# Kernel tuning notes

Hardware: AMD Instinct MI355X
Metric: run time of the kernel (lower is better)

The kernel has to match this reference:

```python
import jax, jax.numpy as jnp
import numpy as np

N = 10000        # nodes
E = 320000       # edges (avg degree 32)
W = 256          # width (assert width >= 256)
H = 8            # num_head (RESCALE_EDGE assumed (1,1) -> nhead=8, dhead=32)
D = W // H       # per-head dim
BOND = 33        # EMBED_BOND[0]
BAG = 3          # indices per edge bag
EPS_GN = 1e-5


def setup_inputs() -> dict:
    key = jax.random.key(0)
    ks = jax.random.split(key, 12)
    x = jax.random.normal(ks[0], (N, W), dtype=jnp.float32)
    edge_idx = jax.random.randint(ks[1], (2, E), 0, N)
    edge_attr = jax.random.randint(ks[2], (E, BAG), 0, BOND)
    # node in-degree wrt scatter target edge_idx[1], clamped to >= 1
    deg = jax.ops.segment_sum(jnp.ones((E,), jnp.float32), edge_idx[1], num_segments=N)
    deg = jnp.maximum(deg, 1.0)
    s = 1.0 / np.sqrt(W)
    W_src = jax.random.normal(ks[3], (W, W), dtype=jnp.float32) * s
    W_tgt = jax.random.normal(ks[4], (W, W), dtype=jnp.float32) * s
    emb = jax.random.normal(ks[5], (BOND, W), dtype=jnp.float32) * 0.02
    emb = emb.at[0].set(0.0)  # padding_idx=0 row is zeros
    sd = 1.0 / np.sqrt(D)
    W_gate = jax.random.normal(ks[6], (H, D, D), dtype=jnp.float32) * sd  # grouped conv1d k=1
    W_val = jax.random.normal(ks[7], (H, D, D), dtype=jnp.float32) * sd
    W_post = jax.random.normal(ks[8], (W, W), dtype=jnp.float32) * s
    deg_param = jnp.zeros((W,), jnp.float32) - 0.01  # DegreeLayer degree_init
    return {"x": x, "deg": deg, "edge_idx": edge_idx, "edge_attr": edge_attr,
            "W_src": W_src, "W_tgt": W_tgt, "emb": emb,
            "W_gate": W_gate, "W_val": W_val, "W_post": W_post,
            "deg_param": deg_param}


def reference(x, deg, edge_idx, edge_attr, W_src, W_tgt, emb, W_gate, W_val, W_post, deg_param):
    # src/tgt 1x1 Conv1d == per-node linear, then edge gather
    xs = x @ W_src.T                      # [N, W]
    xt = x @ W_tgt.T                      # [N, W]
    xx = xs[edge_idx[0]] + xt[edge_idx[1]]  # [E, W]

    # EmbeddingBag(mode='mean', padding_idx=0): padded entries excluded
    mask = (edge_attr != 0).astype(xx.dtype)            # [E, BAG]
    bag = jnp.einsum('ebc,eb->ec', emb[edge_attr], mask)  # [E, W]
    cnt = jnp.maximum(mask.sum(-1, keepdims=True), 1.0)
    gate_bias = bag / cnt

    # GroupNorm(H, W, affine=False) over [E, W, 1]
    xg = xx.reshape(-1, H, D)
    mu = xg.mean(-1, keepdims=True)
    var = xg.var(-1, keepdims=True)
    xn = (xg - mu) / jnp.sqrt(var + EPS_GN)              # [E, H, D]

    # gated grouped 1x1 convs (dropout is identity at eval)
    gin = xn + gate_bias.reshape(-1, H, D)
    gate = jax.nn.relu(jnp.einsum('ehd,hfd->ehf', gin, W_gate))
    val = jnp.einsum('ehd,hfd->ehf', xn, W_val)
    act = (gate * val).reshape(-1, W)                    # [E, W]
    out_e = act @ W_post.T                               # [E, W]

    # scatter-sum to nodes, then degree rescale
    agg = jax.ops.segment_sum(out_e, edge_idx[1], num_segments=x.shape[0])
    return jnp.power(deg[:, None], deg_param) * agg      # [N, W]
```

## Files before the change

kernel.cpp:

```cpp
#include <hip/hip_runtime.h>

#define WID 256
#define EPS_GN 1e-5f

typedef __bf16 v8bf __attribute__((ext_vector_type(8)));
typedef __bf16 v2bf __attribute__((ext_vector_type(2)));
typedef float  v4f  __attribute__((ext_vector_type(4)));

__device__ inline unsigned short f2b(float f) {
    unsigned int u = __builtin_bit_cast(unsigned int, f);
    unsigned int r = (u + 0x7fffu + ((u >> 16) & 1u)) >> 16;
    return (unsigned short)r;
}
__device__ inline float lo16(unsigned int u) { return __builtin_bit_cast(float, u << 16); }
__device__ inline float hi16(unsigned int u) { return __builtin_bit_cast(float, u & 0xffff0000u); }

#if __has_builtin(__builtin_amdgcn_cvt_pk_bf16_f32)
__device__ inline unsigned int pkbf(float a, float b) {
    v2bf r = __builtin_amdgcn_cvt_pk_bf16_f32(a, b);
    return __builtin_bit_cast(unsigned int, r);
}
#else
__device__ inline unsigned int pkbf(float a, float b) {
    return (unsigned int)f2b(a) | ((unsigned int)f2b(b) << 16);
}
#endif

#if __has_builtin(__builtin_amdgcn_fdot2_f32_bf16)
__device__ inline float pairsum(unsigned int u, float s) {
    v2bf p = __builtin_bit_cast(v2bf, u);
    v2bf ones = __builtin_bit_cast(v2bf, 0x3f803f80u);
    return __builtin_amdgcn_fdot2_f32_bf16(p, ones, s, false);
}
#else
__device__ inline float pairsum(unsigned int u, float s) {
    return s + lo16(u) + hi16(u);
}
#endif

__global__ void cast_k(const float* __restrict__ Wsrc, const float* __restrict__ Wtgt,
                       const float* __restrict__ Wp, const float* __restrict__ Wg,
                       const float* __restrict__ Wv, const float* __restrict__ emb,
                       unsigned short* __restrict__ Wsb, unsigned short* __restrict__ Wtb,
                       unsigned short* __restrict__ Wpb, unsigned short* __restrict__ Wgb,
                       unsigned short* __restrict__ Wvb, unsigned short* __restrict__ embWgT,
                       int* __restrict__ cnt, int N, int BOND) {
    int i = blockIdx.x * 256 + threadIdx.x;
    int gsz = gridDim.x * 256;
    for (int j = i; j < N; j += gsz) cnt[j] = 0;
    for (int j = i; j < 65536; j += gsz) {
        Wsb[j] = f2b(Wsrc[j]); Wtb[j] = f2b(Wtgt[j]); Wpb[j] = f2b(Wp[j]);
    }
    for (int j = i; j < 8192; j += gsz) { Wgb[j] = f2b(Wg[j]); Wvb[j] = f2b(Wv[j]); }
    for (int j = i; j < 16384; j += gsz) {
        int jr = j >> 6, k = j & 63;
        float sacc = 0.f;
        if (k < BOND) {
            int h = jr >> 5, f = jr & 31;
            const float* er = emb + (size_t)k * WID + h * 32;
            const float* wr = Wg + h * 1024 + f * 32;
#pragma unroll
            for (int d = 0; d < 32; d++) sacc += er[d] * wr[d];
        }
        embWgT[jr * 64 + k] = f2b(sacc);
    }
}

__global__ __launch_bounds__(256, 2)
void prepproj_k(const float* __restrict__ x, const unsigned short* __restrict__ Wsb,
                const unsigned short* __restrict__ Wtb, const int* __restrict__ eidx,
                unsigned short* __restrict__ xsb, unsigned short* __restrict__ xtb,
                int* __restrict__ cnt, float* __restrict__ aggact,
                int N, int E, int PB, int AUX) {
    __shared__ unsigned short ab[32 * 264];
    int t = threadIdx.x, b = blockIdx.x;

    if (b >= PB) {
        int atid = (b - PB) * 256 + t, asz = AUX * 256;
        {
            float4* ap = (float4*)aggact;
            int n4 = (N * WID) >> 2;
            for (int i = atid; i < n4; i += asz) ap[i] = make_float4(0.f, 0.f, 0.f, 0.f);
        }
        for (int i = atid; i < E; i += asz) atomicAdd(&cnt[eidx[E + i]], 1);
        return;
    }

    int n0 = b * 32;
#pragma unroll
    for (int ch = 0; ch < 8; ch++) {
        int flat = ch * 1024 + t * 4;
        int row = flat >> 8, col = flat & 255;
        int n = n0 + row;
        float4 v = (n < N) ? *(const float4*)&x[(size_t)n * WID + col]
                           : make_float4(0.f, 0.f, 0.f, 0.f);
        *(uint2*)&ab[row * 264 + col] = make_uint2(pkbf(v.x, v.y), pkbf(v.z, v.w));
    }
    __syncthreads();
    int w = t >> 6, lane = t & 63, m = lane & 15, kg = lane >> 4;
#pragma unroll
    for (int pass = 0; pass < 2; pass++) {
        const unsigned short* Wb = pass ? Wtb : Wsb;
        unsigned short* outp = pass ? xtb : xsb;
        v4f acc[2][4];
#pragma unroll
        for (int mt = 0; mt < 2; mt++)
#pragma unroll
            for (int nt = 0; nt < 4; nt++) acc[mt][nt] = (v4f){0.f, 0.f, 0.f, 0.f};
#pragma unroll
        for (int kt = 0; kt < 8; kt++) {
            int k0 = kt * 32 + kg * 8;
            v8bf a0 = *(const v8bf*)&ab[m * 264 + k0];
            v8bf a1 = *(const v8bf*)&ab[(16 + m) * 264 + k0];
#pragma unroll
            for (int nt = 0; nt < 4; nt++) {
                int j = w * 64 + nt * 16 + m;
                v8bf bfr = *(const v8bf*)&Wb[j * 256 + k0];
                acc[0][nt] = __builtin_amdgcn_mfma_f32_16x16x32_bf16(a0, bfr, acc[0][nt], 0, 0, 0);
                acc[1][nt] = __builtin_amdgcn_mfma_f32_16x16x32_bf16(a1, bfr, acc[1][nt], 0, 0, 0);
            }
        }
#pragma unroll
        for (int mt = 0; mt < 2; mt++)
#pragma unroll
            for (int r = 0; r < 4; r++) {
                int n = n0 + mt * 16 + kg * 4 + r;
                if (n < N)
#pragma unroll
                    for (int nt = 0; nt < 4; nt++)
                        outp[(size_t)n * WID + w * 64 + nt * 16 + m] = f2b(acc[mt][nt][r]);
            }
    }
}

__global__ void scan_k(const int* __restrict__ cnt, int* __restrict__ cur, int N) {
    __shared__ int buf[10240];
    __shared__ int part[1024];
    int t = threadIdx.x;
    int C = (N + 1023) >> 10;
    int M = C << 10;
    for (int i = t; i < M; i += 1024) buf[i] = (i < N) ? cnt[i] : 0;
    __syncthreads();
    int base0 = t * C;
    int s = 0;
    for (int i = 0; i < C; i++) s += buf[base0 + i];
    part[t] = s;
    __syncthreads();
    for (int d = 1; d < 1024; d <<= 1) {
        int v = (t >= d) ? part[t - d] : 0;
        __syncthreads();
        part[t] += v;
        __syncthreads();
    }
    int base = (t == 0) ? 0 : part[t - 1];
    for (int i = 0; i < C; i++) {
        int idx = base0 + i;
        int v = buf[idx];
        buf[idx] = base;
        base += v;
    }
    __syncthreads();
    for (int i = t; i < N; i += 1024) cur[i] = buf[i];
}

__global__ void scat_k(const int* __restrict__ eidx, int* __restrict__ cur,
                       int* __restrict__ perm, int E) {
    int i = blockIdx.x * 256 + threadIdx.x;
    if (i < E) { int p = atomicAdd(&cur[eidx[E + i]], 1); perm[p] = i; }
}

__global__ __launch_bounds__(256, 7)
void edge_k(const unsigned short* __restrict__ xsb, const unsigned short* __restrict__ xtb,
            const int* __restrict__ eidx, const int* __restrict__ eattr,
            const int* __restrict__ perm, const unsigned short* __restrict__ Wgb,
            const unsigned short* __restrict__ Wvb, const unsigned short* __restrict__ embWgT,
            float* __restrict__ aggact, int E, int NT, int PER) {
    __shared__ unsigned short xxb[8704];
    __shared__ unsigned short Mld[32 * 72];
    __shared__ int src_s[32], tgt_s[32];
    __shared__ int segmask_s;

    int tile = (blockIdx.x & 7) * PER + (blockIdx.x >> 3);
    if (tile >= NT) return;
    int t = threadIdx.x;
    int e0 = tile * 32;
    int ne = min(32, E - e0);

    {
        int tgtv = -1;
        if (t < 32) {
            int p = (t < ne) ? perm[e0 + t] : -1;
            src_s[t] = (p >= 0) ? eidx[p] : 0;
            tgtv = (p >= 0) ? eidx[E + p] : -1;
            tgt_s[t] = (tgtv >= 0) ? tgtv : 0;
            int a0 = 0, a1 = 0, a2 = 0;
            if (p >= 0) {
                const int* ap = eattr + (size_t)p * 3;
                a0 = ap[0]; a1 = ap[1]; a2 = ap[2];
            }
            unsigned int* Mr = (unsigned int*)&Mld[t * 72];
#pragma unroll
            for (int q = 0; q < 32; q++) Mr[q] = 0;
            int c = (a0 != 0) + (a1 != 0) + (a2 != 0);
            float inv = (p >= 0 && c > 0) ? 1.f / (float)c : 0.f;
            float wa = inv * (float)(1 + (a1 == a0) + (a2 == a0));
            float wb = inv * (float)(1 + (a2 == a1));
            Mld[t * 72 + a0] = f2b(wa);
            if (a1 != a0) Mld[t * 72 + a1] = f2b(wb);
            if (a2 != a0 && a2 != a1) Mld[t * 72 + a2] = f2b(inv);
        }
        if (t < 64) {
            int nxt = __shfl_down(tgtv, 1);
            bool flag = (t < ne) && ((t == ne - 1) || (nxt != tgtv));
            unsigned long long bal = __ballot(flag);
            if (t == 0) segmask_s = (int)(unsigned int)bal;
        }
    }
    __syncthreads();

    {
        int e = t >> 3, c = t & 7;
        int sn = src_s[e], g = tgt_s[e];
        bool live = (e < ne);
        const uint4* ps = (const uint4*)(xsb + (size_t)sn * WID);
        const uint4* pt = (const uint4*)(xtb + (size_t)g * WID);
        uint4 us[4], ut[4];
#pragma unroll
        for (int i = 0; i < 4; i++) { us[i] = ps[c + 8 * i]; ut[i] = pt[c + 8 * i]; }
        float v[4][8], sum[4], sq[4];
#pragma unroll
        for (int i = 0; i < 4; i++) {
            const unsigned int* au = (const unsigned int*)&us[i];
            const unsigned int* bu = (const unsigned int*)&ut[i];
            sum[i] = 0.f; sq[i] = 0.f;
#pragma unroll
            for (int q = 0; q < 4; q++) {
                float x0 = lo16(au[q]) + lo16(bu[q]);
                float x1 = hi16(au[q]) + hi16(bu[q]);
                if (!live) { x0 = 0.f; x1 = 0.f; }
                v[i][2 * q] = x0; v[i][2 * q + 1] = x1;
                sum[i] += x0 + x1;
                sq[i] += x0 * x0 + x1 * x1;
            }
        }
#pragma unroll
        for (int mask = 1; mask <= 2; mask <<= 1)
#pragma unroll
            for (int i = 0; i < 4; i++) {
                sum[i] += __shfl_xor(sum[i], mask);
                sq[i]  += __shfl_xor(sq[i], mask);
            }
#pragma unroll
        for (int i = 0; i < 4; i++) {
            float mu = sum[i] * (1.f / 32.f);
            float var = sq[i] * (1.f / 32.f) - mu * mu;
            float rs = rsqrtf(var + EPS_GN);
            float nmr = -mu * rs;
            unsigned int pk[4];
#pragma unroll
            for (int q = 0; q < 4; q++)
                pk[q] = pkbf(fmaf(v[i][2 * q], rs, nmr), fmaf(v[i][2 * q + 1], rs, nmr));
            *(uint4*)&xxb[e * 264 + (c + 8 * i) * 8] = make_uint4(pk[0], pk[1], pk[2], pk[3]);
        }
    }
    __syncthreads();

    {
        int w = t >> 6, lane = t & 63, m = lane & 15, kg = lane >> 4;
        v8bf axn[2][2], aM[2][2];
#pragma unroll
        for (int mt = 0; mt < 2; mt++) {
            int row = mt * 16 + m;
            axn[0][mt] = *(const v8bf*)&xxb[row * 264 + (w * 2 + 0) * 32 + kg * 8];
            axn[1][mt] = *(const v8bf*)&xxb[row * 264 + (w * 2 + 1) * 32 + kg * 8];
            aM[mt][0] = *(const v8bf*)&Mld[row * 72 + kg * 8];
            aM[mt][1] = *(const v8bf*)&Mld[row * 72 + 32 + kg * 8];
        }
        __syncthreads();
        v4f z = {0.f, 0.f, 0.f, 0.f};
#pragma unroll
        for (int hh = 0; hh < 2; hh++) {
            int h = w * 2 + hh;
#pragma unroll
            for (int nt = 0; nt < 2; nt++) {
                int fj = nt * 16 + m;
                int j = h * 32 + fj;
                v8bf bWg = *(const v8bf*)&Wgb[h * 1024 + fj * 32 + kg * 8];
                v8bf bWv = *(const v8bf*)&Wvb[h * 1024 + fj * 32 + kg * 8];
                v8bf bE0 = *(const v8bf*)&embWgT[j * 64 + kg * 8];
                v8bf bE1 = *(const v8bf*)&embWgT[j * 64 + 32 + kg * 8];
#pragma unroll
                for (int mt = 0; mt < 2; mt++) {
                    v4f cgm = __builtin_amdgcn_mfma_f32_16x16x32_bf16(axn[hh][mt], bWg, z, 0, 0, 0);
                    cgm = __builtin_amdgcn_mfma_f32_16x16x32_bf16(aM[mt][0], bE0, cgm, 0, 0, 0);
                    cgm = __builtin_amdgcn_mfma_f32_16x16x32_bf16(aM[mt][1], bE1, cgm, 0, 0, 0);
                    v4f cv = __builtin_amdgcn_mfma_f32_16x16x32_bf16(axn[hh][mt], bWv, z, 0, 0, 0);
                    float a0 = fmaxf(cgm[0], 0.f) * cv[0];
                    float a1 = fmaxf(cgm[1], 0.f) * cv[1];
                    float a2 = fmaxf(cgm[2], 0.f) * cv[2];
                    float a3 = fmaxf(cgm[3], 0.f) * cv[3];
                    int e0i = mt * 16 + kg * 4;
                    *(unsigned int*)&xxb[j * 34 + e0i]     = pkbf(a0, a1);
                    *(unsigned int*)&xxb[j * 34 + e0i + 2] = pkbf(a2, a3);
                }
            }
        }
    }
    __syncthreads();

    {
        unsigned int mask = (unsigned int)__builtin_amdgcn_readfirstlane(segmask_s);
        float sum = 0.f;
#pragma unroll
        for (int i = 0; i < 16; i++) {
            unsigned int r = *(const unsigned int*)&xxb[t * 34 + 2 * i];
            if (!((mask >> (2 * i)) & 1)) {
                sum = pairsum(r, sum);
                if ((mask >> (2 * i + 1)) & 1) {
                    int tg = __builtin_amdgcn_readfirstlane(tgt_s[2 * i + 1]);
                    atomicAdd(&aggact[(size_t)tg * WID + t], sum);
                    sum = 0.f;
                }
            } else {
                sum += lo16(r);
                int tg = __builtin_amdgcn_readfirstlane(tgt_s[2 * i]);
                atomicAdd(&aggact[(size_t)tg * WID + t], sum);
                sum = hi16(r);
                if ((mask >> (2 * i + 1)) & 1) {
                    int tg2 = __builtin_amdgcn_readfirstlane(tgt_s[2 * i + 1]);
                    atomicAdd(&aggact[(size_t)tg2 * WID + t], sum);
                    sum = 0.f;
                }
            }
        }
    }
}

__global__ __launch_bounds__(256, 2)
void post_k(const float* __restrict__ aggact, const unsigned short* __restrict__ Wpb,
            const float* __restrict__ deg, const float* __restrict__ dp,
            float* __restrict__ out, int N) {
    __shared__ unsigned short ab[32 * 264];
    __shared__ float degl[32];
    int t = threadIdx.x;
    int n0 = blockIdx.x * 32;
#pragma unroll
    for (int ch = 0; ch < 8; ch++) {
        int flat = ch * 1024 + t * 4;
        int row = flat >> 8, col = flat & 255;
        int n = n0 + row;
        float4 v = (n < N) ? *(const float4*)&aggact[(size_t)n * WID + col]
                           : make_float4(0.f, 0.f, 0.f, 0.f);
        *(uint2*)&ab[row * 264 + col] = make_uint2(pkbf(v.x, v.y), pkbf(v.z, v.w));
    }
    if (t < 32) {
        int n = n0 + t;
        degl[t] = (n < N) ? log2f(deg[n]) : 0.f;
    }
    __syncthreads();
    int w = t >> 6, lane = t & 63, m = lane & 15, kg = lane >> 4;
    v4f acc[2][4];
#pragma unroll
    for (int mt = 0; mt < 2; mt++)
#pragma unroll
        for (int nt = 0; nt < 4; nt++) acc[mt][nt] = (v4f){0.f, 0.f, 0.f, 0.f};
#pragma unroll
    for (int kt = 0; kt < 8; kt++) {
        int k0 = kt * 32 + kg * 8;
        v8bf a0 = *(const v8bf*)&ab[m * 264 + k0];
        v8bf a1 = *(const v8bf*)&ab[(16 + m) * 264 + k0];
#pragma unroll
        for (int nt = 0; nt < 4; nt++) {
            int j = w * 64 + nt * 16 + m;
            v8bf b = *(const v8bf*)&Wpb[j * 256 + k0];
            acc[0][nt] = __builtin_amdgcn_mfma_f32_16x16x32_bf16(a0, b, acc[0][nt], 0, 0, 0);
            acc[1][nt] = __builtin_amdgcn_mfma_f32_16x16x32_bf16(a1, b, acc[1][nt], 0, 0, 0);
        }
    }
    float dpv[4];
#pragma unroll
    for (int nt = 0; nt < 4; nt++) dpv[nt] = dp[w * 64 + nt * 16 + m];
#pragma unroll
    for (int mt = 0; mt < 2; mt++)
#pragma unroll
        for (int r = 0; r < 4; r++) {
            int row = mt * 16 + kg * 4 + r;
            int n = n0 + row;
            if (n < N) {
                float ld = degl[row];
#pragma unroll
                for (int nt = 0; nt < 4; nt++)
                    out[(size_t)n * WID + w * 64 + nt * 16 + m] =
                        exp2f(dpv[nt] * ld) * acc[mt][nt][r];
            }
        }
}

extern "C" void kernel_launch(void* const* d_in, const int* in_sizes, int n_in,
                              void* d_out, int out_size, void* d_ws, size_t ws_size,
                              hipStream_t stream) {
    const float* x    = (const float*)d_in[0];
    const float* deg  = (const float*)d_in[1];
    const int*   eidx = (const int*)d_in[2];
    const int*   eatt = (const int*)d_in[3];
    const float* Wsrc = (const float*)d_in[4];
    const float* Wtgt = (const float*)d_in[5];
    const float* emb  = (const float*)d_in[6];
    const float* Wg   = (const float*)d_in[7];
    const float* Wv   = (const float*)d_in[8];
    const float* Wp   = (const float*)d_in[9];
    const float* dp   = (const float*)d_in[10];
    int N = in_sizes[0] / WID;
    int E = in_sizes[2] / 2;
    int BOND = in_sizes[6] / WID;

    float* ws     = (float*)d_ws;
    float* aggact = ws;
    int*   cnt    = (int*)(aggact + (size_t)N * WID);
    int*   cur    = cnt + N;
    int*   perm   = cur + N;
    unsigned short* xsb = (unsigned short*)(perm + E);
    unsigned short* xtb = xsb + (size_t)N * WID;
    unsigned short* Wsb = xtb + (size_t)N * WID;
    unsigned short* Wtb = Wsb + 65536;
    unsigned short* Wpb = Wtb + 65536;
    unsigned short* Wgb = Wpb + 65536;
    unsigned short* Wvb = Wgb + 8192;
    unsigned short* embWgT = Wvb + 8192;

    int PB = (N + 31) / 32;
    int AUX = 128;
    int NT = (E + 31) / 32;
    int PER = (NT + 7) / 8;

    cast_k<<<320, 256, 0, stream>>>(Wsrc, Wtgt, Wp, Wg, Wv, emb,
                                    Wsb, Wtb, Wpb, Wgb, Wvb, embWgT, cnt, N, BOND);
    prepproj_k<<<PB + AUX, 256, 0, stream>>>(x, Wsb, Wtb, eidx, xsb, xtb, cnt, aggact,
                                             N, E, PB, AUX);
    scan_k<<<1, 1024, 0, stream>>>(cnt, cur, N);
    scat_k<<<(E + 255) / 256, 256, 0, stream>>>(eidx, cur, perm, E);
    edge_k<<<PER * 8, 256, 0, stream>>>(xsb, xtb, eidx, eatt, perm, Wgb, Wvb, embWgT,
                                        aggact, E, NT, PER);
    post_k<<<(N + 31) / 32, 256, 0, stream>>>(aggact, Wpb, deg, dp, (float*)d_out, N);
}
```

Baseline: 230.3 us.

## Pre-sort edge data in scatter, fold bond embedding to 32 slots, vectorize stores

The scatter kernel now writes src, tgt and packed bag attributes directly in target-sorted order, so the edge kernel reads them contiguously instead of chasing a permutation through the edge arrays. The bond-embedding projection table is folded from 64 to 32 columns by aliasing index 32 to slot 0 (the padding slot), which drops one MFMA per gate tile and halves the embedding LDS tile. The projection and post GEMMs swap their MFMA operands so each lane holds four consecutive columns, giving packed 8-byte bf16 and float4 output stores. Occupancy is raised to 8 and the pad edges are zeroed in setup. The fold depends on BOND being at most 33, and pad edges now rely on zeroed buffers instead of the old liveness masking.

```diff
diff --git a/kernel.cpp b/kernel.cpp
--- a/kernel.cpp
+++ b/kernel.cpp
@@ -44,25 +44,29 @@
                        unsigned short* __restrict__ Wsb, unsigned short* __restrict__ Wtb,
                        unsigned short* __restrict__ Wpb, unsigned short* __restrict__ Wgb,
                        unsigned short* __restrict__ Wvb, unsigned short* __restrict__ embWgT,
-                       int* __restrict__ cnt, int N, int BOND) {
+                       int* __restrict__ cnt, int* __restrict__ ssrc,
+                       int* __restrict__ stgt, int* __restrict__ sattr,
+                       int N, int BOND, int E, int NT32) {
     int i = blockIdx.x * 256 + threadIdx.x;
     int gsz = gridDim.x * 256;
     for (int j = i; j < N; j += gsz) cnt[j] = 0;
+    for (int j = E + i; j < NT32; j += gsz) { ssrc[j] = 0; stgt[j] = 0; sattr[j] = 0; }
     for (int j = i; j < 65536; j += gsz) {
         Wsb[j] = f2b(Wsrc[j]); Wtb[j] = f2b(Wtgt[j]); Wpb[j] = f2b(Wp[j]);
     }
     for (int j = i; j < 8192; j += gsz) { Wgb[j] = f2b(Wg[j]); Wvb[j] = f2b(Wv[j]); }
-    for (int j = i; j < 16384; j += gsz) {
-        int jr = j >> 6, k = j & 63;
+    for (int j = i; j < 8192; j += gsz) {
+        int jr = j >> 5, k = j & 31;
+        int kk = k ? k : 32;
         float sacc = 0.f;
-        if (k < BOND) {
+        if (kk < BOND) {
             int h = jr >> 5, f = jr & 31;
-            const float* er = emb + (size_t)k * WID + h * 32;
+            const float* er = emb + (size_t)kk * WID + h * 32;
             const float* wr = Wg + h * 1024 + f * 32;
 #pragma unroll
             for (int d = 0; d < 32; d++) sacc += er[d] * wr[d];
         }
-        embWgT[jr * 64 + k] = f2b(sacc);
+        embWgT[jr * 32 + k] = f2b(sacc);
     }
 }
 
@@ -116,20 +120,23 @@
             for (int nt = 0; nt < 4; nt++) {
                 int j = w * 64 + nt * 16 + m;
                 v8bf bfr = *(const v8bf*)&Wb[j * 256 + k0];
-                acc[0][nt] = __builtin_amdgcn_mfma_f32_16x16x32_bf16(a0, bfr, acc[0][nt], 0, 0, 0);
-                acc[1][nt] = __builtin_amdgcn_mfma_f32_16x16x32_bf16(a1, bfr, acc[1][nt], 0, 0, 0);
-            }
-        }
-#pragma unroll
-        for (int mt = 0; mt < 2; mt++)
-#pragma unroll
-            for (int r = 0; r < 4; r++) {
-                int n = n0 + mt * 16 + kg * 4 + r;
-                if (n < N)
-#pragma unroll
-                    for (int nt = 0; nt < 4; nt++)
-                        outp[(size_t)n * WID + w * 64 + nt * 16 + m] = f2b(acc[mt][nt][r]);
-            }
+                acc[0][nt] = __builtin_amdgcn_mfma_f32_16x16x32_bf16(bfr, a0, acc[0][nt], 0, 0, 0);
+                acc[1][nt] = __builtin_amdgcn_mfma_f32_16x16x32_bf16(bfr, a1, acc[1][nt], 0, 0, 0);
+            }
+        }
+#pragma unroll
+        for (int mt = 0; mt < 2; mt++) {
+            int n = n0 + mt * 16 + m;
+            if (n < N) {
+#pragma unroll
+                for (int nt = 0; nt < 4; nt++) {
+                    int j0 = w * 64 + nt * 16 + kg * 4;
+                    *(uint2*)&outp[(size_t)n * WID + j0] =
+                        make_uint2(pkbf(acc[mt][nt][0], acc[mt][nt][1]),
+                                   pkbf(acc[mt][nt][2], acc[mt][nt][3]));
+                }
+            }
+        }
     }
 }
 
@@ -163,20 +170,28 @@
     for (int i = t; i < N; i += 1024) cur[i] = buf[i];
 }
 
-__global__ void scat_k(const int* __restrict__ eidx, int* __restrict__ cur,
-                       int* __restrict__ perm, int E) {
+__global__ void scat_k(const int* __restrict__ eidx, const int* __restrict__ eattr,
+                       int* __restrict__ cur, int* __restrict__ ssrc,
+                       int* __restrict__ stgt, int* __restrict__ sattr, int E) {
     int i = blockIdx.x * 256 + threadIdx.x;
-    if (i < E) { int p = atomicAdd(&cur[eidx[E + i]], 1); perm[p] = i; }
-}
-
-__global__ __launch_bounds__(256, 7)
+    if (i < E) {
+        int tg = eidx[E + i];
+        int p = atomicAdd(&cur[tg], 1);
+        ssrc[p] = eidx[i];
+        stgt[p] = tg;
+        const int* ap = eattr + (size_t)i * 3;
+        sattr[p] = (ap[0] & 63) | ((ap[1] & 63) << 6) | ((ap[2] & 63) << 12);
+    }
+}
+
+__global__ __launch_bounds__(256, 8)
 void edge_k(const unsigned short* __restrict__ xsb, const unsigned short* __restrict__ xtb,
-            const int* __restrict__ eidx, const int* __restrict__ eattr,
-            const int* __restrict__ perm, const unsigned short* __restrict__ Wgb,
+            const int* __restrict__ ssrc, const int* __restrict__ stgt,
+            const int* __restrict__ sattr, const unsigned short* __restrict__ Wgb,
             const unsigned short* __restrict__ Wvb, const unsigned short* __restrict__ embWgT,
             float* __restrict__ aggact, int E, int NT, int PER) {
     __shared__ unsigned short xxb[8704];
-    __shared__ unsigned short Mld[32 * 72];
+    __shared__ unsigned short Mld[32 * 40];
     __shared__ int src_s[32], tgt_s[32];
     __shared__ int segmask_s;
 
@@ -189,25 +204,23 @@
     {
         int tgtv = -1;
         if (t < 32) {
-            int p = (t < ne) ? perm[e0 + t] : -1;
-            src_s[t] = (p >= 0) ? eidx[p] : 0;
-            tgtv = (p >= 0) ? eidx[E + p] : -1;
-            tgt_s[t] = (tgtv >= 0) ? tgtv : 0;
-            int a0 = 0, a1 = 0, a2 = 0;
-            if (p >= 0) {
-                const int* ap = eattr + (size_t)p * 3;
-                a0 = ap[0]; a1 = ap[1]; a2 = ap[2];
-            }
-            unsigned int* Mr = (unsigned int*)&Mld[t * 72];
-#pragma unroll
-            for (int q = 0; q < 32; q++) Mr[q] = 0;
+            int e = e0 + t;
+            src_s[t] = ssrc[e];
+            int tg = stgt[e];
+            tgt_s[t] = tg;
+            int pa = sattr[e];
+            unsigned int* Mr = (unsigned int*)&Mld[t * 40];
+#pragma unroll
+            for (int q = 0; q < 16; q++) Mr[q] = 0;
+            int a0 = pa & 63, a1 = (pa >> 6) & 63, a2 = (pa >> 12) & 63;
             int c = (a0 != 0) + (a1 != 0) + (a2 != 0);
-            float inv = (p >= 0 && c > 0) ? 1.f / (float)c : 0.f;
+            float inv = (c > 0) ? 1.f / (float)c : 0.f;
             float wa = inv * (float)(1 + (a1 == a0) + (a2 == a0));
             float wb = inv * (float)(1 + (a2 == a1));
-            Mld[t * 72 + a0] = f2b(wa);
-            if (a1 != a0) Mld[t * 72 + a1] = f2b(wb);
-            if (a2 != a0 && a2 != a1) Mld[t * 72 + a2] = f2b(inv);
+            if (a0) Mld[t * 40 + (a0 & 31)] = f2b(wa);
+            if (a1 && a1 != a0) Mld[t * 40 + (a1 & 31)] = f2b(wb);
+            if (a2 && a2 != a0 && a2 != a1) Mld[t * 40 + (a2 & 31)] = f2b(inv);
+            tgtv = (t < ne) ? tg : -1;
         }
         if (t < 64) {
             int nxt = __shfl_down(tgtv, 1);
@@ -221,7 +234,6 @@
     {
         int e = t >> 3, c = t & 7;
         int sn = src_s[e], g = tgt_s[e];
-        bool live = (e < ne);
         const uint4* ps = (const uint4*)(xsb + (size_t)sn * WID);
         const uint4* pt = (const uint4*)(xtb + (size_t)g * WID);
         uint4 us[4], ut[4];
@@ -237,7 +249,6 @@
             for (int q = 0; q < 4; q++) {
                 float x0 = lo16(au[q]) + lo16(bu[q]);
                 float x1 = hi16(au[q]) + hi16(bu[q]);
-                if (!live) { x0 = 0.f; x1 = 0.f; }
                 v[i][2 * q] = x0; v[i][2 * q + 1] = x1;
                 sum[i] += x0 + x1;
                 sq[i] += x0 * x0 + x1 * x1;
@@ -267,14 +278,13 @@
 
     {
         int w = t >> 6, lane = t & 63, m = lane & 15, kg = lane >> 4;
-        v8bf axn[2][2], aM[2][2];
+        v8bf axn[2][2], aM[2];
 #pragma unroll
         for (int mt = 0; mt < 2; mt++) {
             int row = mt * 16 + m;
             axn[0][mt] = *(const v8bf*)&xxb[row * 264 + (w * 2 + 0) * 32 + kg * 8];
             axn[1][mt] = *(const v8bf*)&xxb[row * 264 + (w * 2 + 1) * 32 + kg * 8];
-            aM[mt][0] = *(const v8bf*)&Mld[row * 72 + kg * 8];
-            aM[mt][1] = *(const v8bf*)&Mld[row * 72 + 32 + kg * 8];
+            aM[mt] = *(const v8bf*)&Mld[row * 40 + kg * 8];
         }
         __syncthreads();
         v4f z = {0.f, 0.f, 0.f, 0.f};
@@ -287,13 +297,11 @@
                 int j = h * 32 + fj;
                 v8bf bWg = *(const v8bf*)&Wgb[h * 1024 + fj * 32 + kg * 8];
                 v8bf bWv = *(const v8bf*)&Wvb[h * 1024 + fj * 32 + kg * 8];
-                v8bf bE0 = *(const v8bf*)&embWgT[j * 64 + kg * 8];
-                v8bf bE1 = *(const v8bf*)&embWgT[j * 64 + 32 + kg * 8];
+                v8bf bE  = *(const v8bf*)&embWgT[j * 32 + kg * 8];
 #pragma unroll
                 for (int mt = 0; mt < 2; mt++) {
                     v4f cgm = __builtin_amdgcn_mfma_f32_16x16x32_bf16(axn[hh][mt], bWg, z, 0, 0, 0);
-                    cgm = __builtin_amdgcn_mfma_f32_16x16x32_bf16(aM[mt][0], bE0, cgm, 0, 0, 0);
-                    cgm = __builtin_amdgcn_mfma_f32_16x16x32_bf16(aM[mt][1], bE1, cgm, 0, 0, 0);
+                    cgm = __builtin_amdgcn_mfma_f32_16x16x32_bf16(aM[mt], bE, cgm, 0, 0, 0);
                     v4f cv = __builtin_amdgcn_mfma_f32_16x16x32_bf16(axn[hh][mt], bWv, z, 0, 0, 0);
                     float a0 = fmaxf(cgm[0], 0.f) * cv[0];
                     float a1 = fmaxf(cgm[1], 0.f) * cv[1];
@@ -373,27 +381,28 @@
         for (int nt = 0; nt < 4; nt++) {
             int j = w * 64 + nt * 16 + m;
             v8bf b = *(const v8bf*)&Wpb[j * 256 + k0];
-            acc[0][nt] = __builtin_amdgcn_mfma_f32_16x16x32_bf16(a0, b, acc[0][nt], 0, 0, 0);
-            acc[1][nt] = __builtin_amdgcn_mfma_f32_16x16x32_bf16(a1, b, acc[1][nt], 0, 0, 0);
-        }
-    }
-    float dpv[4];
-#pragma unroll
-    for (int nt = 0; nt < 4; nt++) dpv[nt] = dp[w * 64 + nt * 16 + m];
-#pragma unroll
-    for (int mt = 0; mt < 2; mt++)
-#pragma unroll
-        for (int r = 0; r < 4; r++) {
-            int row = mt * 16 + kg * 4 + r;
-            int n = n0 + row;
-            if (n < N) {
-                float ld = degl[row];
-#pragma unroll
-                for (int nt = 0; nt < 4; nt++)
-                    out[(size_t)n * WID + w * 64 + nt * 16 + m] =
-                        exp2f(dpv[nt] * ld) * acc[mt][nt][r];
-            }
-        }
+            acc[0][nt] = __builtin_amdgcn_mfma_f32_16x16x32_bf16(b, a0, acc[0][nt], 0, 0, 0);
+            acc[1][nt] = __builtin_amdgcn_mfma_f32_16x16x32_bf16(b, a1, acc[1][nt], 0, 0, 0);
+        }
+    }
+#pragma unroll
+    for (int mt = 0; mt < 2; mt++) {
+        int n = n0 + mt * 16 + m;
+        if (n < N) {
+            float ld = degl[mt * 16 + m];
+#pragma unroll
+            for (int nt = 0; nt < 4; nt++) {
+                int j0 = w * 64 + nt * 16 + kg * 4;
+                float4 dv = *(const float4*)&dp[j0];
+                float4 o;
+                o.x = exp2f(dv.x * ld) * acc[mt][nt][0];
+                o.y = exp2f(dv.y * ld) * acc[mt][nt][1];
+                o.z = exp2f(dv.z * ld) * acc[mt][nt][2];
+                o.w = exp2f(dv.w * ld) * acc[mt][nt][3];
+                *(float4*)&out[(size_t)n * WID + j0] = o;
+            }
+        }
+    }
 }
 
 extern "C" void kernel_launch(void* const* d_in, const int* in_sizes, int n_in,
@@ -414,12 +423,17 @@
     int E = in_sizes[2] / 2;
     int BOND = in_sizes[6] / WID;
 
+    int NT = (E + 31) / 32;
+    int NT32 = NT * 32;
+
     float* ws     = (float*)d_ws;
     float* aggact = ws;
     int*   cnt    = (int*)(aggact + (size_t)N * WID);
     int*   cur    = cnt + N;
-    int*   perm   = cur + N;
-    unsigned short* xsb = (unsigned short*)(perm + E);
+    int*   ssrc   = cur + N;
+    int*   stgt   = ssrc + NT32;
+    int*   sattr  = stgt + NT32;
+    unsigned short* xsb = (unsigned short*)(sattr + NT32);
     unsigned short* xtb = xsb + (size_t)N * WID;
     unsigned short* Wsb = xtb + (size_t)N * WID;
     unsigned short* Wtb = Wsb + 65536;
@@ -430,16 +444,16 @@
 
     int PB = (N + 31) / 32;
     int AUX = 128;
-    int NT = (E + 31) / 32;
     int PER = (NT + 7) / 8;
 
     cast_k<<<320, 256, 0, stream>>>(Wsrc, Wtgt, Wp, Wg, Wv, emb,
-                                    Wsb, Wtb, Wpb, Wgb, Wvb, embWgT, cnt, N, BOND);
+                                    Wsb, Wtb, Wpb, Wgb, Wvb, embWgT,
+                                    cnt, ssrc, stgt, sattr, N, BOND, E, NT32);
     prepproj_k<<<PB + AUX, 256, 0, stream>>>(x, Wsb, Wtb, eidx, xsb, xtb, cnt, aggact,
                                              N, E, PB, AUX);
     scan_k<<<1, 1024, 0, stream>>>(cnt, cur, N);
-    scat_k<<<(E + 255) / 256, 256, 0, stream>>>(eidx, cur, perm, E);
-    edge_k<<<PER * 8, 256, 0, stream>>>(xsb, xtb, eidx, eatt, perm, Wgb, Wvb, embWgT,
+    scat_k<<<(E + 255) / 256, 256, 0, stream>>>(eidx, eatt, cur, ssrc, stgt, sattr, E);
+    edge_k<<<PER * 8, 256, 0, stream>>>(xsb, xtb, ssrc, stgt, sattr, Wgb, Wvb, embWgT,
                                         aggact, E, NT, PER);
     post_k<<<(N + 31) / 32, 256, 0, stream>>>(aggact, Wpb, deg, dp, (float*)d_out, N);
 }
```

Result: faster. 216.3 us (-6.1%).
